# Kernel optimization log

Hardware: AMD Instinct MI355X
Metric: run time of the kernel (lower is better)

The kernel has to match this reference:

```python
import jax, jax.numpy as jnp
import numpy as np

EPS = 1e-08
TEMPERATURE = 1.0
HEADS = 4
OUT_DIM = 32
IN_DIM = 128
N_NODES = 100000
N_EDGES = 1600000


def setup_inputs() -> dict:
    key = jax.random.key(0)
    k1, k2, k3, k4, k5, k6 = jax.random.split(key, 6)
    x = jax.random.normal(k1, (N_NODES, IN_DIM), dtype=jnp.float32)
    # nn.Linear(in_dim, heads*out_dim, bias=False).weight -> [heads*out_dim, in_dim]
    W = jax.random.normal(k2, (HEADS * OUT_DIM, IN_DIM), dtype=jnp.float32) * 0.05
    a_src = jax.random.normal(k3, (HEADS, OUT_DIM), dtype=jnp.float32) * 0.1
    a_dst = jax.random.normal(k4, (HEADS, OUT_DIM), dtype=jnp.float32) * 0.1
    edge_index = jax.random.randint(k5, (2, N_EDGES), 0, N_NODES, dtype=jnp.int32)
    rnbrw_weights = jax.random.uniform(k6, (N_EDGES,), dtype=jnp.float32)
    return {"x": x, "W": W, "a_src": a_src, "a_dst": a_dst,
            "edge_index": edge_index, "rnbrw_weights": rnbrw_weights}


def reference(x, W, a_src, a_dst, edge_index, rnbrw_weights):
    N = x.shape[0]
    heads, out_dim = a_src.shape
    # h = W(x).view(N, heads, out_dim)
    h = (x @ W.T).reshape(N, heads, out_dim)
    src, dst = edge_index[0], edge_index[1]
    h_src = h[src]  # [E, heads, out_dim]
    h_dst = h[dst]  # [E, heads, out_dim]
    # per-edge attention scores [E, heads]
    score = jnp.einsum('ehd,hd->eh', h_src, a_src) + jnp.einsum('ehd,hd->eh', h_dst, a_dst)
    # strategy == 'pre_softmax_bias'
    score = score + jnp.log(rnbrw_weights + EPS)[:, None]
    score = jnp.where(score >= 0, score, 0.2 * score)  # leaky_relu(0.2)
    scaled = score / TEMPERATURE
    # edge softmax over incoming edges of each dst node
    seg_max = jax.ops.segment_max(scaled, dst, num_segments=N)      # [N, heads]
    exp_s = jnp.exp(scaled - seg_max[dst])                           # [E, heads]
    denom = jax.ops.segment_sum(exp_s, dst, num_segments=N)         # [N, heads]
    alpha = exp_s / (denom[dst] + EPS)                               # [E, heads]
    # scatter-add aggregation: out[dst] += alpha * h_src
    out = jax.ops.segment_sum(alpha[..., None] * h_src, dst, num_segments=N)
    out = out.reshape(N, heads * out_dim)
    return out, alpha
```

## Files before the change

### kernel.cpp

```cpp
#include <hip/hip_runtime.h>

#define EPS 1e-8f

__device__ inline unsigned short f2bf(float f) {
    unsigned u = __float_as_uint(f);
    unsigned r = u + 0x7fffu + ((u >> 16) & 1u);
    return (unsigned short)(r >> 16);
}
__device__ inline float bflo(unsigned v) { return __uint_as_float(v << 16); }
__device__ inline float bfhi(unsigned v) { return __uint_as_float(v & 0xffff0000u); }

__global__ __launch_bounds__(256) void gemm_count_kernel(
    const float* __restrict__ x, const float* __restrict__ W,
    const float* __restrict__ a_src, const float* __restrict__ a_dst,
    unsigned short* __restrict__ hb, float* __restrict__ s_src, float* __restrict__ s_dst,
    int N, int n_tiles,
    const int* __restrict__ dst, int* __restrict__ counts, int E)
{
    __shared__ float Wt[128 * 64];
    __shared__ float xt[128 * 64];

    const int bid = blockIdx.x;
    const int r3  = bid % 3;

    if (r3 == 2) {
        const int c = bid / 3;
        for (int e = c * 256 + threadIdx.x; e < E; e += 512 * 256)
            atomicAdd(counts + dst[e], 1);
        return;
    }

    const int g    = (bid / 3) * 2 + r3;
    const int half = g >> 9;
    const int bx   = g & 511;
    const int t    = threadIdx.x;
    const float* Wh = W + half * 64 * 128;

#pragma unroll
    for (int p = 0; p < 8; ++p) {
        int idx = p * 256 + t;
        int ol = (idx & 31) | ((idx >> 10) << 5);
        int k4 = (idx >> 5) & 31;
        float4 w = *(const float4*)(Wh + ol * 128 + k4 * 4);
        Wt[(4 * k4 + 0) * 64 + ol] = w.x;
        Wt[(4 * k4 + 1) * 64 + ol] = w.y;
        Wt[(4 * k4 + 2) * 64 + ol] = w.z;
        Wt[(4 * k4 + 3) * 64 + ol] = w.w;
    }

    const int o4 = t & 15;
    const int n4g = t >> 4;
    const int head = half * 2 + (o4 >> 3);
    const float4 as = *(const float4*)(a_src + head * 32 + (o4 & 7) * 4);
    const float4 ad = *(const float4*)(a_dst + head * 32 + (o4 & 7) * 4);

    float4 xr[8];

    {
        const int nbase = bx * 64;
#pragma unroll
        for (int p = 0; p < 8; ++p) {
            int idx = p * 256 + t;
            int n = idx & 63;
            int k4 = idx >> 6;
            int ng = nbase + n;
            xr[p] = make_float4(0.f, 0.f, 0.f, 0.f);
            if (bx < n_tiles && ng < N)
                xr[p] = *(const float4*)(x + (size_t)ng * 128 + k4 * 4);
        }
    }

    for (int tile = bx; tile < n_tiles; tile += 512) {
        const int nbase = tile * 64;
        __syncthreads();
#pragma unroll
        for (int p = 0; p < 8; ++p) {
            int idx = p * 256 + t;
            int n = idx & 63;
            int k4 = idx >> 6;
            xt[(4 * k4 + 0) * 64 + n] = xr[p].x;
            xt[(4 * k4 + 1) * 64 + n] = xr[p].y;
            xt[(4 * k4 + 2) * 64 + n] = xr[p].z;
            xt[(4 * k4 + 3) * 64 + n] = xr[p].w;
        }
        __syncthreads();

        {
            int nt2 = tile + 512;
            if (nt2 < n_tiles) {
                const int nb2 = nt2 * 64;
#pragma unroll
                for (int p = 0; p < 8; ++p) {
                    int idx = p * 256 + t;
                    int n = idx & 63;
                    int k4 = idx >> 6;
                    int ng = nb2 + n;
                    xr[p] = make_float4(0.f, 0.f, 0.f, 0.f);
                    if (ng < N)
                        xr[p] = *(const float4*)(x + (size_t)ng * 128 + k4 * 4);
                }
            }
        }

        float acc[4][4];
#pragma unroll
        for (int i = 0; i < 4; ++i)
#pragma unroll
            for (int j = 0; j < 4; ++j) acc[i][j] = 0.f;

        for (int k = 0; k < 128; ++k) {
            float4 wv = *(const float4*)(Wt + k * 64 + 4 * o4);
            float4 xv = *(const float4*)(xt + k * 64 + 4 * n4g);
            float wa[4] = {wv.x, wv.y, wv.z, wv.w};
            float xa[4] = {xv.x, xv.y, xv.z, xv.w};
#pragma unroll
            for (int i = 0; i < 4; ++i)
#pragma unroll
                for (int j = 0; j < 4; ++j) acc[i][j] += xa[i] * wa[j];
        }

#pragma unroll
        for (int i = 0; i < 4; ++i) {
            int n = nbase + 4 * n4g + i;
            float ps = acc[i][0] * as.x + acc[i][1] * as.y + acc[i][2] * as.z + acc[i][3] * as.w;
            float pd = acc[i][0] * ad.x + acc[i][1] * ad.y + acc[i][2] * ad.z + acc[i][3] * ad.w;
            ps += __shfl_xor(ps, 1); ps += __shfl_xor(ps, 2); ps += __shfl_xor(ps, 4);
            pd += __shfl_xor(pd, 1); pd += __shfl_xor(pd, 2); pd += __shfl_xor(pd, 4);
            if (n < N) {
                ushort4 hv;
                hv.x = f2bf(acc[i][0]); hv.y = f2bf(acc[i][1]);
                hv.z = f2bf(acc[i][2]); hv.w = f2bf(acc[i][3]);
                *(ushort4*)(hb + (size_t)n * 128 + half * 64 + 4 * o4) = hv;
                if ((o4 & 7) == 0) {
                    s_src[n * 4 + head] = ps;
                    s_dst[n * 4 + head] = pd;
                }
            }
        }
    }
}

__global__ __launch_bounds__(256) void scan1_kernel(
    const int* __restrict__ counts, int* __restrict__ offs, int* __restrict__ bsum, int N)
{
    __shared__ int sh[256];
    int t = threadIdx.x;
    int base = blockIdx.x * 1024 + t * 4;
    int c[4];
#pragma unroll
    for (int j = 0; j < 4; ++j) c[j] = (base + j < N) ? counts[base + j] : 0;
    int tsum = c[0] + c[1] + c[2] + c[3];
    sh[t] = tsum;
    __syncthreads();
    for (int off = 1; off < 256; off <<= 1) {
        int v = (t >= off) ? sh[t - off] : 0;
        __syncthreads();
        sh[t] += v;
        __syncthreads();
    }
    int run = sh[t] - tsum;
    if (t == 255) bsum[blockIdx.x] = sh[255];
#pragma unroll
    for (int j = 0; j < 4; ++j) {
        if (base + j < N) { offs[base + j] = run; run += c[j]; }
    }
}

__global__ __launch_bounds__(512) void scan2_kernel(int* __restrict__ bsum, int nb)
{
    __shared__ int sh[512];
    int t = threadIdx.x;
    if (nb <= 512) {
        int v = (t < nb) ? bsum[t] : 0;
        sh[t] = v;
        __syncthreads();
        for (int off = 1; off < 512; off <<= 1) {
            int u = (t >= off) ? sh[t - off] : 0;
            __syncthreads();
            sh[t] += u;
            __syncthreads();
        }
        if (t < nb) bsum[t] = sh[t] - v;
    } else if (t == 0) {
        int acc = 0;
        for (int i = 0; i < nb; ++i) { int v = bsum[i]; bsum[i] = acc; acc += v; }
    }
}

__global__ __launch_bounds__(256) void scan3_kernel(
    int* __restrict__ offs, const int* __restrict__ bsum,
    int* __restrict__ cursor, int N)
{
    int i = blockIdx.x * 256 + threadIdx.x;
    if (i >= N) return;
    int v = offs[i] + bsum[i >> 10];
    offs[i] = v;
    cursor[i] = v;
}

__global__ __launch_bounds__(256) void scatter_kernel(
    const int* __restrict__ src, const int* __restrict__ dst,
    const float* __restrict__ rnbrw,
    int* __restrict__ cursor, int2* __restrict__ rec,
    int E, int ssz, int bps)
{
    const int shard = blockIdx.x & 7;
    const int j = blockIdx.x >> 3;
    const int lo = shard * ssz;
    const int hi = lo + ssz;
    const int stride = bps * 1024;
    for (int base = j * 1024; base < E; base += stride) {
        int e0 = base + threadIdx.x * 4;
        if (e0 + 3 < E) {
            int4 d4 = *(const int4*)(dst + e0);
            int da[4] = {d4.x, d4.y, d4.z, d4.w};
#pragma unroll
            for (int c = 0; c < 4; ++c) {
                int d = da[c];
                if (d >= lo && d < hi) {
                    int e = e0 + c;
                    float lw = __logf(rnbrw[e] + EPS);
                    int pos = atomicAdd(cursor + d, 1);
                    rec[pos] = make_int2(src[e], __float_as_int(lw));
                }
            }
        } else {
            for (int e = e0; e < E; ++e) {
                int d = dst[e];
                if (d >= lo && d < hi) {
                    float lw = __logf(rnbrw[e] + EPS);
                    int pos = atomicAdd(cursor + d, 1);
                    rec[pos] = make_int2(src[e], __float_as_int(lw));
                }
            }
        }
    }
}

__global__ __launch_bounds__(256) void node_aggr_kernel(
    const int* __restrict__ offs, const int* __restrict__ counts,
    const int2* __restrict__ rec,
    const float* __restrict__ s_src, const float* __restrict__ s_dst,
    const unsigned short* __restrict__ hb,
    float* __restrict__ inv_den, float* __restrict__ out, int N)
{
    int gid = blockIdx.x * 256 + threadIdx.x;
    int n = gid >> 5;
    int l = gid & 31;
    if (n >= N) return;

    const int q    = l & 15;
    const int half = l >> 4;
    const int head = q >> 2;

    const int beg = offs[n];
    const int cnt = counts[n];
    const float sdn = s_dst[n * 4 + head];

    float a0 = 0.f, a1 = 0.f, a2 = 0.f, a3 = 0.f;
    float a4 = 0.f, a5 = 0.f, a6 = 0.f, a7 = 0.f;
    float den = 0.f;

    for (int i = 0; i < cnt; i += 4) {
        int j0 = i + half;
        int j1 = i + 2 + half;
        int jc0 = (j0 < cnt) ? j0 : 0;
        int jc1 = (j1 < cnt) ? j1 : 0;
        int2 r0 = rec[(size_t)beg + jc0];
        int2 r1 = rec[(size_t)beg + jc1];
        uint4 v0 = *(const uint4*)(hb + (size_t)r0.x * 128 + q * 8);
        uint4 v1 = *(const uint4*)(hb + (size_t)r1.x * 128 + q * 8);
        float t0 = s_src[(size_t)r0.x * 4 + head] + sdn + __int_as_float(r0.y);
        float t1 = s_src[(size_t)r1.x * 4 + head] + sdn + __int_as_float(r1.y);
        t0 = (t0 >= 0.f) ? t0 : 0.2f * t0;
        t1 = (t1 >= 0.f) ? t1 : 0.2f * t1;
        float e0 = __expf(t0);
        float e1 = __expf(t1);
        if (j0 >= cnt) e0 = 0.f;
        if (j1 >= cnt) e1 = 0.f;
        a0 += e0 * bflo(v0.x); a1 += e0 * bfhi(v0.x);
        a2 += e0 * bflo(v0.y); a3 += e0 * bfhi(v0.y);
        a4 += e0 * bflo(v0.z); a5 += e0 * bfhi(v0.z);
        a6 += e0 * bflo(v0.w); a7 += e0 * bfhi(v0.w);
        a0 += e1 * bflo(v1.x); a1 += e1 * bfhi(v1.x);
        a2 += e1 * bflo(v1.y); a3 += e1 * bfhi(v1.y);
        a4 += e1 * bflo(v1.z); a5 += e1 * bfhi(v1.z);
        a6 += e1 * bflo(v1.w); a7 += e1 * bfhi(v1.w);
        den += e0 + e1;
    }

    a0 += __shfl_xor(a0, 16, 32); a1 += __shfl_xor(a1, 16, 32);
    a2 += __shfl_xor(a2, 16, 32); a3 += __shfl_xor(a3, 16, 32);
    a4 += __shfl_xor(a4, 16, 32); a5 += __shfl_xor(a5, 16, 32);
    a6 += __shfl_xor(a6, 16, 32); a7 += __shfl_xor(a7, 16, 32);
    den += __shfl_xor(den, 16, 32);

    const float inv = 1.f / (den + EPS);

    float d0 = __shfl(den, 0, 32);
    float d1 = __shfl(den, 4, 32);
    float d2 = __shfl(den, 8, 32);
    float d3 = __shfl(den, 12, 32);

    float4 o = half ? make_float4(a4 * inv, a5 * inv, a6 * inv, a7 * inv)
                    : make_float4(a0 * inv, a1 * inv, a2 * inv, a3 * inv);
    *(float4*)(out + (size_t)n * 128 + q * 8 + half * 4) = o;

    if (l == 0)
        *(float4*)(inv_den + (size_t)n * 4) =
            make_float4(1.f / (d0 + EPS), 1.f / (d1 + EPS),
                        1.f / (d2 + EPS), 1.f / (d3 + EPS));
}

__global__ __launch_bounds__(256) void alpha_kernel(
    const int* __restrict__ src, const int* __restrict__ dst,
    const float* __restrict__ rnbrw,
    const float* __restrict__ s_src, const float* __restrict__ s_dst,
    const float* __restrict__ inv_den, float* __restrict__ alpha, int E)
{
    int e = blockIdx.x * 256 + threadIdx.x;
    if (e >= E) return;
    int s = src[e], d = dst[e];
    float lw = __logf(rnbrw[e] + EPS);
    float4 a = *(const float4*)(s_src + s * 4);
    float4 b = *(const float4*)(s_dst + d * 4);
    float4 iv = *(const float4*)(inv_den + (size_t)d * 4);
    float4 al;
    float v;
    v = a.x + b.x + lw; v = (v >= 0.f) ? v : 0.2f * v; al.x = __expf(v) * iv.x;
    v = a.y + b.y + lw; v = (v >= 0.f) ? v : 0.2f * v; al.y = __expf(v) * iv.y;
    v = a.z + b.z + lw; v = (v >= 0.f) ? v : 0.2f * v; al.z = __expf(v) * iv.z;
    v = a.w + b.w + lw; v = (v >= 0.f) ? v : 0.2f * v; al.w = __expf(v) * iv.w;
    *(float4*)(alpha + (size_t)e * 4) = al;
}

extern "C" void kernel_launch(void* const* d_in, const int* in_sizes, int n_in,
                              void* d_out, int out_size, void* d_ws, size_t ws_size,
                              hipStream_t stream) {
    const float* x      = (const float*)d_in[0];
    const float* W      = (const float*)d_in[1];
    const float* a_src  = (const float*)d_in[2];
    const float* a_dst  = (const float*)d_in[3];
    const int*   eidx   = (const int*)d_in[4];
    const float* rnbrw  = (const float*)d_in[5];

    const int E = in_sizes[5];
    const int N = in_sizes[0] / 128;

    float* out   = (float*)d_out;
    float* alpha = out + (size_t)N * 128;

    char* w = (char*)d_ws;
    unsigned short* hb = (unsigned short*)w;  w += (size_t)N * 128 * 2;
    int2* rec     = (int2*)w;                 w += (size_t)E * 8;
    float* s_src  = (float*)w;                w += (size_t)N * 16;
    float* s_dst  = (float*)w;                w += (size_t)N * 16;
    float* inv_den = (float*)w;               w += (size_t)N * 16;
    int* counts  = (int*)w;                   w += (size_t)N * 4;
    int* offs    = (int*)w;                   w += (size_t)N * 4;
    int* cursor  = (int*)w;                   w += (size_t)N * 4;
    int* bsum    = (int*)w;                   w += 512 * 4;

    const int* src = eidx;
    const int* dst = eidx + E;

    hipMemsetAsync(counts, 0, (size_t)N * sizeof(int), stream);

    int n_tiles = (N + 63) / 64;
    gemm_count_kernel<<<1536, 256, 0, stream>>>(
        x, W, a_src, a_dst, hb, s_src, s_dst, N, n_tiles, dst, counts, E);

    int nb = (N + 1023) / 1024;
    scan1_kernel<<<nb, 256, 0, stream>>>(counts, offs, bsum, N);
    scan2_kernel<<<1, 512, 0, stream>>>(bsum, nb);
    scan3_kernel<<<(N + 255) / 256, 256, 0, stream>>>(offs, bsum, cursor, N);

    int ssz = (N + 7) / 8;
    int bps = 256;
    scatter_kernel<<<8 * bps, 256, 0, stream>>>(src, dst, rnbrw, cursor, rec, E, ssz, bps);

    int ablocks = ((size_t)N * 32 + 255) / 256;
    node_aggr_kernel<<<ablocks, 256, 0, stream>>>(offs, counts, rec, s_src, s_dst, hb,
                                                  inv_den, out, N);

    int eblocks = (E + 255) / 256;
    alpha_kernel<<<eblocks, 256, 0, stream>>>(src, dst, rnbrw, s_src, s_dst,
                                              inv_den, alpha, E);
}
```

Baseline: 384.7 us.

## Enlarge GEMM tile to 256 nodes with 8x8 register blocking and K-chunked staging

Replaces the persistent 64-node-tile GEMM loop with one 256-node tile per block, where each thread computes an 8x8 output block instead of 4x4. The x tile is staged through shared memory in 16-wide K chunks with register prefetch of the next chunk. The intent is more FMAs per shared-memory load and less LDS traffic. It costs more registers (64 accumulators), handled with a launch_bounds occupancy hint, and drops the persistent-loop overlap across tiles.

New measurement: 385.8 us. About the same (+0.3%).

```diff
diff --git a/kernel.cpp b/kernel.cpp
--- a/kernel.cpp
+++ b/kernel.cpp
@@ -10,7 +10,7 @@
 __device__ inline float bflo(unsigned v) { return __uint_as_float(v << 16); }
 __device__ inline float bfhi(unsigned v) { return __uint_as_float(v & 0xffff0000u); }
 
-__global__ __launch_bounds__(256) void gemm_count_kernel(
+__global__ __launch_bounds__(256, 3) void gemm_count_kernel(
     const float* __restrict__ x, const float* __restrict__ W,
     const float* __restrict__ a_src, const float* __restrict__ a_dst,
     unsigned short* __restrict__ hb, float* __restrict__ s_src, float* __restrict__ s_dst,
@@ -18,7 +18,7 @@
     const int* __restrict__ dst, int* __restrict__ counts, int E)
 {
     __shared__ float Wt[128 * 64];
-    __shared__ float xt[128 * 64];
+    __shared__ float xt[16 * 256];
 
     const int bid = blockIdx.x;
     const int r3  = bid % 3;
@@ -30,10 +30,12 @@
         return;
     }
 
-    const int g    = (bid / 3) * 2 + r3;
-    const int half = g >> 9;
-    const int bx   = g & 511;
-    const int t    = threadIdx.x;
+    const int g = (bid / 3) * 2 + r3;
+    if (g >= 2 * n_tiles) return;
+    const int half  = (g >= n_tiles) ? 1 : 0;
+    const int tile  = g - half * n_tiles;
+    const int nbase = tile * 256;
+    const int t     = threadIdx.x;
     const float* Wh = W + half * 64 * 128;
 
 #pragma unroll
@@ -48,93 +50,96 @@
         Wt[(4 * k4 + 3) * 64 + ol] = w.w;
     }
 
-    const int o4 = t & 15;
-    const int n4g = t >> 4;
-    const int head = half * 2 + (o4 >> 3);
-    const float4 as = *(const float4*)(a_src + head * 32 + (o4 & 7) * 4);
-    const float4 ad = *(const float4*)(a_dst + head * 32 + (o4 & 7) * 4);
-
-    float4 xr[8];
-
+    const int og = t & 7;
+    const int ng = t >> 3;
+    const int head = half * 2 + (og >> 2);
+    const float4 as0 = *(const float4*)(a_src + head * 32 + (og & 3) * 8);
+    const float4 as1 = *(const float4*)(a_src + head * 32 + (og & 3) * 8 + 4);
+    const float4 ad0 = *(const float4*)(a_dst + head * 32 + (og & 3) * 8);
+    const float4 ad1 = *(const float4*)(a_dst + head * 32 + (og & 3) * 8 + 4);
+
+    float acc[8][8];
+#pragma unroll
+    for (int i = 0; i < 8; ++i)
+#pragma unroll
+        for (int j = 0; j < 8; ++j) acc[i][j] = 0.f;
+
+    float4 xr[4];
     {
-        const int nbase = bx * 64;
-#pragma unroll
-        for (int p = 0; p < 8; ++p) {
+#pragma unroll
+        for (int p = 0; p < 4; ++p) {
             int idx = p * 256 + t;
-            int n = idx & 63;
-            int k4 = idx >> 6;
-            int ng = nbase + n;
+            int kq = idx & 3;
+            int n  = idx >> 2;
+            int ngl = nbase + n;
             xr[p] = make_float4(0.f, 0.f, 0.f, 0.f);
-            if (bx < n_tiles && ng < N)
-                xr[p] = *(const float4*)(x + (size_t)ng * 128 + k4 * 4);
-        }
-    }
-
-    for (int tile = bx; tile < n_tiles; tile += 512) {
-        const int nbase = tile * 64;
-        __syncthreads();
-#pragma unroll
-        for (int p = 0; p < 8; ++p) {
+            if (ngl < N)
+                xr[p] = *(const float4*)(x + (size_t)ngl * 128 + kq * 4);
+        }
+    }
+
+    for (int c = 0; c < 8; ++c) {
+        __syncthreads();
+#pragma unroll
+        for (int p = 0; p < 4; ++p) {
             int idx = p * 256 + t;
-            int n = idx & 63;
-            int k4 = idx >> 6;
-            xt[(4 * k4 + 0) * 64 + n] = xr[p].x;
-            xt[(4 * k4 + 1) * 64 + n] = xr[p].y;
-            xt[(4 * k4 + 2) * 64 + n] = xr[p].z;
-            xt[(4 * k4 + 3) * 64 + n] = xr[p].w;
-        }
-        __syncthreads();
-
-        {
-            int nt2 = tile + 512;
-            if (nt2 < n_tiles) {
-                const int nb2 = nt2 * 64;
-#pragma unroll
-                for (int p = 0; p < 8; ++p) {
-                    int idx = p * 256 + t;
-                    int n = idx & 63;
-                    int k4 = idx >> 6;
-                    int ng = nb2 + n;
-                    xr[p] = make_float4(0.f, 0.f, 0.f, 0.f);
-                    if (ng < N)
-                        xr[p] = *(const float4*)(x + (size_t)ng * 128 + k4 * 4);
-                }
+            int kq = idx & 3;
+            int n  = idx >> 2;
+            xt[(kq * 4 + 0) * 256 + n] = xr[p].x;
+            xt[(kq * 4 + 1) * 256 + n] = xr[p].y;
+            xt[(kq * 4 + 2) * 256 + n] = xr[p].z;
+            xt[(kq * 4 + 3) * 256 + n] = xr[p].w;
+        }
+        __syncthreads();
+
+        if (c < 7) {
+            const int kb2 = (c + 1) * 16;
+#pragma unroll
+            for (int p = 0; p < 4; ++p) {
+                int idx = p * 256 + t;
+                int kq = idx & 3;
+                int n  = idx >> 2;
+                int ngl = nbase + n;
+                xr[p] = make_float4(0.f, 0.f, 0.f, 0.f);
+                if (ngl < N)
+                    xr[p] = *(const float4*)(x + (size_t)ngl * 128 + kb2 + kq * 4);
             }
         }
 
-        float acc[4][4];
-#pragma unroll
-        for (int i = 0; i < 4; ++i)
-#pragma unroll
-            for (int j = 0; j < 4; ++j) acc[i][j] = 0.f;
-
-        for (int k = 0; k < 128; ++k) {
-            float4 wv = *(const float4*)(Wt + k * 64 + 4 * o4);
-            float4 xv = *(const float4*)(xt + k * 64 + 4 * n4g);
-            float wa[4] = {wv.x, wv.y, wv.z, wv.w};
-            float xa[4] = {xv.x, xv.y, xv.z, xv.w};
-#pragma unroll
-            for (int i = 0; i < 4; ++i)
-#pragma unroll
-                for (int j = 0; j < 4; ++j) acc[i][j] += xa[i] * wa[j];
-        }
-
-#pragma unroll
-        for (int i = 0; i < 4; ++i) {
-            int n = nbase + 4 * n4g + i;
-            float ps = acc[i][0] * as.x + acc[i][1] * as.y + acc[i][2] * as.z + acc[i][3] * as.w;
-            float pd = acc[i][0] * ad.x + acc[i][1] * ad.y + acc[i][2] * ad.z + acc[i][3] * ad.w;
-            ps += __shfl_xor(ps, 1); ps += __shfl_xor(ps, 2); ps += __shfl_xor(ps, 4);
-            pd += __shfl_xor(pd, 1); pd += __shfl_xor(pd, 2); pd += __shfl_xor(pd, 4);
-            if (n < N) {
-                ushort4 hv;
-                hv.x = f2bf(acc[i][0]); hv.y = f2bf(acc[i][1]);
-                hv.z = f2bf(acc[i][2]); hv.w = f2bf(acc[i][3]);
-                *(ushort4*)(hb + (size_t)n * 128 + half * 64 + 4 * o4) = hv;
-                if ((o4 & 7) == 0) {
-                    s_src[n * 4 + head] = ps;
-                    s_dst[n * 4 + head] = pd;
-                }
+        const int kb = c * 16;
+        for (int k = 0; k < 16; ++k) {
+            float4 wv0 = *(const float4*)(Wt + (kb + k) * 64 + og * 8);
+            float4 wv1 = *(const float4*)(Wt + (kb + k) * 64 + og * 8 + 4);
+            float4 xv0 = *(const float4*)(xt + k * 256 + ng * 8);
+            float4 xv1 = *(const float4*)(xt + k * 256 + ng * 8 + 4);
+            float wa[8] = {wv0.x, wv0.y, wv0.z, wv0.w, wv1.x, wv1.y, wv1.z, wv1.w};
+            float xa[8] = {xv0.x, xv0.y, xv0.z, xv0.w, xv1.x, xv1.y, xv1.z, xv1.w};
+#pragma unroll
+            for (int i = 0; i < 8; ++i)
+#pragma unroll
+                for (int j = 0; j < 8; ++j) acc[i][j] += xa[i] * wa[j];
+        }
+    }
+
+#pragma unroll
+    for (int i = 0; i < 8; ++i) {
+        int n = nbase + ng * 8 + i;
+        float ps = acc[i][0] * as0.x + acc[i][1] * as0.y + acc[i][2] * as0.z + acc[i][3] * as0.w
+                 + acc[i][4] * as1.x + acc[i][5] * as1.y + acc[i][6] * as1.z + acc[i][7] * as1.w;
+        float pd = acc[i][0] * ad0.x + acc[i][1] * ad0.y + acc[i][2] * ad0.z + acc[i][3] * ad0.w
+                 + acc[i][4] * ad1.x + acc[i][5] * ad1.y + acc[i][6] * ad1.z + acc[i][7] * ad1.w;
+        ps += __shfl_xor(ps, 1); ps += __shfl_xor(ps, 2);
+        pd += __shfl_xor(pd, 1); pd += __shfl_xor(pd, 2);
+        if (n < N) {
+            uint4 hv;
+            hv.x = (unsigned)f2bf(acc[i][0]) | ((unsigned)f2bf(acc[i][1]) << 16);
+            hv.y = (unsigned)f2bf(acc[i][2]) | ((unsigned)f2bf(acc[i][3]) << 16);
+            hv.z = (unsigned)f2bf(acc[i][4]) | ((unsigned)f2bf(acc[i][5]) << 16);
+            hv.w = (unsigned)f2bf(acc[i][6]) | ((unsigned)f2bf(acc[i][7]) << 16);
+            *(uint4*)(hb + (size_t)n * 128 + half * 64 + og * 8) = hv;
+            if ((og & 3) == 0) {
+                s_src[n * 4 + head] = ps;
+                s_dst[n * 4 + head] = pd;
             }
         }
     }
@@ -366,7 +371,7 @@
 
     hipMemsetAsync(counts, 0, (size_t)N * sizeof(int), stream);
 
-    int n_tiles = (N + 63) / 64;
+    int n_tiles = (N + 255) / 256;
     gemm_count_kernel<<<1536, 256, 0, stream>>>(
         x, W, a_src, a_dst, hb, s_src, s_dst, N, n_tiles, dst, counts, E);
 
```
